# Performance work log

Measured on AMD Instinct MI355X. Metric: run time of the kernel, lower is better.

Reference implementation:

```python
import jax, jax.numpy as jnp
import numpy as np

B, M, N, F, H = 4, 512, 1024, 256, 256
K, K2, KC, RADIUS = 8, 4, 16, 0.5
EPS = 1e-5


def _cdist(a, b):
    d2 = (jnp.sum(a * a, -1)[..., :, None] + jnp.sum(b * b, -1)[..., None, :]
          - 2.0 * jnp.einsum('bnd,bmd->bnm', a, b))
    return jnp.sqrt(jnp.maximum(d2, 0.0))


def _scf_oe(xyz):
    # spherical coords (r, theta, phi) relative to cloud centroid -> (B,3,Npts)
    rel = xyz - jnp.mean(xyz, axis=1, keepdims=True)
    r = jnp.sqrt(jnp.sum(rel * rel, -1) + 1e-8)
    theta = jnp.arccos(jnp.clip(rel[..., 2] / r, -1.0, 1.0))
    phi = jnp.arctan2(rel[..., 1], rel[..., 0])
    return jnp.stack([r, theta, phi], axis=1)


def _knn_desc(xyz):
    # per-point SCF descriptor: sorted distances to KC nearest neighbors
    d = _cdist(xyz, xyz)
    return jnp.sort(d, axis=-1)[..., 1:KC + 1]


def _inorm(x):
    # InstanceNorm1d, affine=False: normalize over last dim per (b, row)
    mu = jnp.mean(x, -1, keepdims=True)
    var = jnp.var(x, -1, keepdims=True)
    return (x - mu) / jnp.sqrt(var + EPS)


def _conv1x1(x, W, g, b):
    # Conv2d 1x1 + BN(affine) + ReLU on (B,C,N,K)
    y = jnp.einsum('bcnk,oc->bonk', x, W)
    return jax.nn.relu(g[:, None, None] * y + b[:, None, None])


def _conv12(x, W, g, b):
    # Conv2d kernel (1,2) stride (1,2) + BN(affine) + ReLU on (B,C,N,P)
    Bb, C, Nn, P = x.shape
    xr = x.reshape(Bb, C, Nn, P // 2, 2)
    y = jnp.einsum('bcnpt,oct->bonp', xr, W)
    return jax.nn.relu(g[:, None, None] * y + b[:, None, None])


def _pointsift(xyz, feat, params):
    # PointSIFT OE: nearest neighbor in each of 8 octants within radius
    w1, g1, b1, w2, g2, b2, w3, g3, b3 = params
    Bb, Nn, _ = xyz.shape
    diff = xyz[:, None, :, :] - xyz[:, :, None, :]  # diff[b,i,j] = xyz[j]-xyz[i]
    d2 = jnp.sum(diff * diff, -1)
    octant = ((diff[..., 0] > 0).astype(jnp.int32) * 4
              + (diff[..., 1] > 0).astype(jnp.int32) * 2
              + (diff[..., 2] > 0).astype(jnp.int32))
    base = jnp.broadcast_to(jnp.arange(Nn)[None, :], (Bb, Nn))
    idxs = []
    for c in range(8):  # fixed small structural loop
        m = (octant == c) & (d2 <= RADIUS * RADIUS) & (d2 > 0)
        dm = jnp.where(m, d2, jnp.inf)
        j = jnp.argmin(dm, -1)
        valid = jnp.isfinite(jnp.min(dm, -1))
        idxs.append(jnp.where(valid, j, base))
    idx = jnp.stack(idxs, -1)  # (B,N,8)
    gxyz = jax.vmap(lambda p, i: p[i])(xyz, idx) - xyz[:, :, None, :]
    gfeat = jax.vmap(lambda f, i: f[i])(feat, idx)
    g = jnp.concatenate([gxyz, gfeat], -1).transpose(0, 3, 1, 2)  # (B,3+C,N,8)
    g = _conv12(g, w1, g1, b1)
    g = _conv12(g, w2, g2, b2)
    g = _conv12(g, w3, g3, b3)
    return g[..., 0]  # (B,C,N)


def setup_inputs():
    key = jax.random.key(0)
    ks = iter(jax.random.split(key, 64))
    rn = lambda shape, s=0.05: jax.random.normal(next(ks), shape, dtype=jnp.float32) * s
    ones = lambda shape: jnp.ones(shape, jnp.float32)
    zeros = lambda shape: jnp.zeros(shape, jnp.float32)
    inp = {
        'template_feature': rn((B, F, M), 1.0),
        'search_feature': rn((B, F, N), 1.0),
        'template_xyz': rn((B, M, 3), 1.0),
        'search_xyz': rn((B, N, 3), 1.0),
        'template_bc': rn((B, M, 9), 1.0),
        'search_bc': rn((B, N, 9), 1.0),
        'mlp_w1': rn((H, F + 3)), 'mlp_g1': ones(H), 'mlp_b1': zeros(H),
        'mlp_w2': rn((H, H)), 'mlp_g2': ones(H), 'mlp_b2': zeros(H),
        'mlp_w3': rn((H, H)), 'mlp_g3': ones(H), 'mlp_b3': zeros(H),
        'fea_w1': rn((F, H)), 'fea_g1': ones(F), 'fea_b1': zeros(F),
        'fea_w2': rn((F, F)), 'fea_bias2': zeros(F),
        'attn_wqkv': rn((3 * F, F)),
        'pos_w1': rn((64, 12)), 'pos_b1': zeros(64),
        'pos_w2': rn((F, 64)), 'pos_b2': zeros(F),
        'amlp_w1': rn((4 * F, F)), 'amlp_b1': zeros(4 * F),
        'amlp_w2': rn((F, 4 * F)), 'amlp_b2': zeros(F),
        'oe1_w1': rn((F, F + 3, 2)), 'oe1_g1': ones(F), 'oe1_b1': zeros(F),
        'oe1_w2': rn((F, F, 2)), 'oe1_g2': ones(F), 'oe1_b2': zeros(F),
        'oe1_w3': rn((F, F, 2)), 'oe1_g3': ones(F), 'oe1_b3': zeros(F),
        'oe2_w1': rn((F, F + 3, 2)), 'oe2_g1': ones(F), 'oe2_b1': zeros(F),
        'oe2_w2': rn((F, F, 2)), 'oe2_g2': ones(F), 'oe2_b2': zeros(F),
        'oe2_w3': rn((F, F, 2)), 'oe2_g3': ones(F), 'oe2_b3': zeros(F),
    }
    return inp


def reference(template_feature, search_feature, template_xyz, search_xyz, template_bc, search_bc,
              mlp_w1, mlp_g1, mlp_b1, mlp_w2, mlp_g2, mlp_b2, mlp_w3, mlp_g3, mlp_b3,
              fea_w1, fea_g1, fea_b1, fea_w2, fea_bias2,
              attn_wqkv, pos_w1, pos_b1, pos_w2, pos_b2, amlp_w1, amlp_b1, amlp_w2, amlp_b2,
              oe1_w1, oe1_g1, oe1_b1, oe1_w2, oe1_g2, oe1_b2, oe1_w3, oe1_g3, oe1_b3,
              oe2_w1, oe2_g1, oe2_b1, oe2_w2, oe2_g2, oe2_b2, oe2_w3, oe2_g3, oe2_b3):
    # ---- box-cloud distance + candidate pruning ----
    dist_bc = _cdist(template_bc, search_bc)  # (B,M,N)
    t_box = jnp.concatenate([template_xyz.transpose(0, 2, 1), template_bc.transpose(0, 2, 1),
                             template_feature, _scf_oe(template_xyz)], 1)  # (B,15+F,M)
    s_box = jnp.concatenate([search_xyz.transpose(0, 2, 1), search_bc.transpose(0, 2, 1),
                             search_feature, _scf_oe(search_xyz)], 1)      # (B,15+F,N)
    idx_b = jnp.argsort(dist_bc, axis=1)[:, :3 * K, :].transpose(0, 2, 1)  # (B,N,3K)
    dist_xyz = _cdist(search_xyz, template_xyz)  # (B,N,M)
    bi = jnp.arange(B)[:, None, None]
    ni = jnp.arange(N)[None, :, None]
    mask = jnp.full((B, N, M), 1e5, jnp.float32).at[bi, ni, idx_b].set(1.0)
    idx_k = jnp.argsort((dist_xyz * mask).transpose(0, 2, 1), axis=1)[:, :K, :].transpose(0, 2, 1)  # (B,N,K)
    # ---- SCF descriptor matching restricted to xyz candidates ----
    sd = _knn_desc(search_xyz)
    td = _knn_desc(template_xyz)
    mask2 = jnp.full((B, N, M), 1e5, jnp.float32).at[bi, ni, idx_k].set(1.0)
    dist_scf = _cdist(sd, td) * mask2
    idx_s = jnp.argsort(dist_scf.transpose(0, 2, 1), axis=1)[:, :K2, :].transpose(0, 2, 1)  # (B,N,K2)
    # ---- grouping + shared MLP ----
    corr = jax.vmap(lambda f, i: f[:, i])(t_box, idx_s)        # (B,15+F,N,K2)
    fused = jnp.concatenate([s_box[..., None], corr], -1)      # (B,15+F,N,K2+1)
    feats = fused.transpose(0, 2, 3, 1)[..., 12:]              # drop xyz+bc -> (B,N,K2+1,F+3)
    h = feats.transpose(0, 3, 1, 2)
    h = _conv1x1(h, mlp_w1, mlp_g1, mlp_b1)
    h = _conv1x1(h, mlp_w2, mlp_g2, mlp_b2)
    h = _conv1x1(h, mlp_w3, mlp_g3, mlp_b3)
    h = h.transpose(0, 2, 3, 1)                                # (B,N,K2+1,H)
    nn_xyz = corr[:, 0:3].transpose(0, 2, 3, 1)
    st_xyz = jnp.concatenate([search_xyz[:, :, None, :], nn_xyz], 2)
    nn_bc = corr[:, 3:12].transpose(0, 2, 3, 1)
    st_bc = jnp.concatenate([search_bc[:, :, None, :], nn_bc], 2)
    pos = jnp.concatenate([st_xyz, st_bc], -1)                 # (B,N,K2+1,12)
    KP1 = K2 + 1
    x = h.reshape(B * N, KP1, H)
    p = pos.reshape(B * N, KP1, 12)
    # ---- point transformer layer over tiny neighborhoods ----
    qkv = jnp.einsum('bnd,ed->bne', x, attn_wqkv)
    q, k, v = jnp.split(qkv, 3, axis=-1)
    rel_pos = p[:, :, None, :] - p[:, None, :, :]
    pe = jnp.einsum('bijp,hp->bijh', rel_pos, pos_w1) + pos_b1
    pe = jnp.einsum('bijh,dh->bijd', jax.nn.relu(pe), pos_w2) + pos_b2
    sim_in = q[:, :, None, :] - k[:, None, :, :] + pe
    hh = jax.nn.relu(jnp.einsum('bijd,hd->bijh', sim_in, amlp_w1) + amlp_b1)
    sim = jnp.einsum('bijh,dh->bijd', hh, amlp_w2) + amlp_b2
    attn = jax.nn.softmax(sim, axis=-2)
    agg = jnp.einsum('bijd,bijd->bid', attn, v[:, None, :, :] + pe)
    ff = agg.reshape(B, N, KP1, H).transpose(0, 3, 1, 2)[..., 0]  # (B,F,N)
    # ---- residual + instance norms + fea_layer ----
    ff = ff + search_feature
    ff = _inorm(ff.transpose(0, 2, 1)).transpose(0, 2, 1)
    y = jax.nn.relu(fea_g1[:, None] * jnp.einsum('bcn,oc->bon', ff, fea_w1) + fea_b1[:, None])
    y = jnp.einsum('bcn,oc->bon', y, fea_w2) + fea_bias2[:, None]
    y = _inorm((y + ff).transpose(0, 2, 1)).transpose(0, 2, 1)
    # ---- two PointSIFT OE modules with residuals ----
    y = y + _pointsift(search_xyz, y.transpose(0, 2, 1), (oe1_w1, oe1_g1, oe1_b1, oe1_w2, oe1_g2, oe1_b2, oe1_w3, oe1_g3, oe1_b3))
    y = y + _pointsift(search_xyz, y.transpose(0, 2, 1), (oe2_w1, oe2_g1, oe2_b1, oe2_w2, oe2_g2, oe2_b2, oe2_w3, oe2_g3, oe2_b3))
    return y
```

## Files before the change

kernel.cpp:

```cpp
#include <hip/hip_runtime.h>
#include <hip/hip_bf16.h>
#include <math.h>

constexpr int Bc = 4, Mc = 512, Nc = 1024, Fc = 256;
constexpr int KCc = 16;
constexpr float INFF = 3.0e38f;

typedef __attribute__((ext_vector_type(8))) short short8b;
typedef __attribute__((ext_vector_type(4))) float f32x4;

__device__ __forceinline__ short f2bf(float f) {
  __hip_bfloat16 h = __float2bfloat16(f);
  return *reinterpret_cast<short*>(&h);
}
__device__ __forceinline__ float bf2f(short s) {
  unsigned int u = ((unsigned int)(unsigned short)s) << 16;
  return __uint_as_float(u);
}
__device__ __forceinline__ unsigned long long umin64(unsigned long long a, unsigned long long b) {
  return a < b ? a : b;
}

__device__ __forceinline__ float blk_sum(float v, float* red) {
  int t = threadIdx.x;
// ... 73 lines not shown
  float mx = blk_sum(sx, red) / (float)P;
  float my = blk_sum(sy, red) / (float)P;
  float mz = blk_sum(sz, red) / (float)P;
  for (int i = threadIdx.x; i < P; i += 256) {
    float a = x[3 * i] - mx, c = x[3 * i + 1] - my, d = x[3 * i + 2] - mz;
    float r = sqrtf(a * a + c * c + d * d + 1e-8f);
    float ct = d / r;
    ct = fminf(1.f, fmaxf(-1.f, ct));
    out[((size_t)b * 3 + 0) * P + i] = r;
    out[((size_t)b * 3 + 1) * P + i] = acosf(ct);
    out[((size_t)b * 3 + 2) * P + i] = atan2f(c, a);
  }
}

template <int P>
__global__ __launch_bounds__(256) void knn_kernel(const float* __restrict__ xyz,
                                                  float* __restrict__ desc) {
  constexpr int E = P / 64;
  int wv = threadIdx.x >> 6, l = threadIdx.x & 63;
  int pt = blockIdx.x * 4 + wv;
  int b = pt / P, i = pt % P;
  const float* x = xyz + (size_t)b * P * 3;
  float xi0 = x[3 * i], xi1 = x[3 * i + 1], xi2 = x[3 * i + 2];
  float d2r[E];
#pragma unroll
  for (int q = 0; q < E; ++q) {
    int j = q * 64 + l;
    float dx = x[3 * j] - xi0, dy = x[3 * j + 1] - xi1, dz = x[3 * j + 2] - xi2;
    d2r[q] = dx * dx + dy * dy + dz * dz;
  }
  for (int round = 0; round < KCc + 1; ++round) {
    unsigned long long k = ~0ULL;
#pragma unroll
    for (int q = 0; q < E; ++q) {
      unsigned long long c =
          ((unsigned long long)__float_as_uint(d2r[q]) << 32) | (unsigned)(q * 64 + l);
      k = umin64(k, c);
    }
#pragma unroll
    for (int m = 1; m < 64; m <<= 1) k = umin64(k, __shfl_xor(k, m));
    int widx = (int)(unsigned)k;
    if (round > 0 && l == 0)
      desc[((size_t)b * P + i) * KCc + (round - 1)] = sqrtf(__uint_as_float((unsigned)(k >> 32)));
    if ((widx & 63) == l) {
      int q = widx >> 6;
#pragma unroll
      for (int qq = 0; qq < E; ++qq)
        if (qq == q) d2r[qq] = INFF;
    }
  }
}

__global__ __launch_bounds__(256) void select_kernel(
    const float* __restrict__ tbc, const float* __restrict__ sbc,
    const float* __restrict__ txyz, const float* __restrict__ sxyz,
    const float* __restrict__ sd, const float* __restrict__ td,
    int* __restrict__ idx_s) {
  __shared__ int cand4[4][24];
  int wv = threadIdx.x >> 6, l = threadIdx.x & 63;
  int pt = blockIdx.x * 4 + wv;
  int b = pt / Nc, n = pt % Nc;
  const float* sb = sbc + ((size_t)b * Nc + n) * 9;
  float sreg[9];
#pragma unroll
  for (int c = 0; c < 9; ++c) sreg[c] = sb[c];
  float d2r[8];
#pragma unroll
  for (int q = 0; q < 8; ++q) {
    int m = q * 64 + l;
    const float* tb = tbc + ((size_t)b * Mc + m) * 9;
    float acc = 0.f;
#pragma unroll
    for (int c = 0; c < 9; ++c) { float d = tb[c] - sreg[c]; acc += d * d; }
    d2r[q] = acc;
  }
  for (int round = 0; round < 24; ++round) {
    unsigned long long k = ~0ULL;
#pragma unroll
    for (int q = 0; q < 8; ++q) {
      unsigned long long c =
          ((unsigned long long)__float_as_uint(d2r[q]) << 32) | (unsigned)(q * 64 + l);
      k = umin64(k, c);
    }
#pragma unroll
    for (int m = 1; m < 64; m <<= 1) k = umin64(k, __shfl_xor(k, m));
    int widx = (int)(unsigned)k;
    if (l == 0) cand4[wv][round] = widx;
    if ((widx & 63) == l) {
      int q = widx >> 6;
#pragma unroll
      for (int qq = 0; qq < 8; ++qq)
        if (qq == q) d2r[qq] = INFF;
    }
  }
  if (l == 0) {
    int* cand = cand4[wv];
    const float* sp = sxyz + ((size_t)b * Nc + n) * 3;
    float sx = sp[0], sy = sp[1], sz = sp[2];
    float dv[24];
    for (int t2 = 0; t2 < 24; ++t2) {
      const float* tp = txyz + ((size_t)b * Mc + cand[t2]) * 3;
      float dx = tp[0] - sx, dy = tp[1] - sy, dz = tp[2] - sz;
      dv[t2] = dx * dx + dy * dy + dz * dz;
    }
    int c8[8]; bool used[24];
    for (int t2 = 0; t2 < 24; ++t2) used[t2] = false;
    for (int r = 0; r < 8; ++r) {
      float bv = INFF; int bt = -1, bm = 0x7fffffff;
      for (int t2 = 0; t2 < 24; ++t2) {
        if (used[t2]) continue;
        int m = cand[t2];
        if (bt < 0 || dv[t2] < bv || (dv[t2] == bv && m < bm)) { bv = dv[t2]; bt = t2; bm = m; }
      }
      used[bt] = true; c8[r] = bm;
    }
    const float* sdp = sd + ((size_t)b * Nc + n) * KCc;
    float sdr[16];
    for (int t2 = 0; t2 < 16; ++t2) sdr[t2] = sdp[t2];
    float dscf[8];
    for (int r = 0; r < 8; ++r) {
      const float* tdp = td + ((size_t)b * Mc + c8[r]) * KCc;
      float acc = 0.f;
      for (int t2 = 0; t2 < 16; ++t2) { float d = sdr[t2] - tdp[t2]; acc += d * d; }
      dscf[r] = acc;
    }
    bool u8[8] = {false, false, false, false, false, false, false, false};
    for (int r = 0; r < 4; ++r) {
      float bv = INFF; int bt = -1, bm = 0x7fffffff;
      for (int t2 = 0; t2 < 8; ++t2) {
        if (u8[t2]) continue;
        if (bt < 0 || dscf[t2] < bv || (dscf[t2] == bv && c8[t2] < bm)) { bv = dscf[t2]; bt = t2; bm = c8[t2]; }
      }
      u8[bt] = true;
      idx_s[(((size_t)b * Nc + n) << 2) + r] = bm;
    }
  }
}

__global__ __launch_bounds__(512, 4) void mlp_attn_kernel(
    const float* __restrict__ sfeatT, const float* __restrict__ tfeatT,
    const float* __restrict__ sscf, const float* __restrict__ tscf,
    const int* __restrict__ idx_s,
    const short* __restrict__ mw1f, const float* __restrict__ mg1, const float* __restrict__ mb1,
    const short* __restrict__ mw2f, const float* __restrict__ mg2, const float* __restrict__ mb2,
    const short* __restrict__ mw3f, const float* __restrict__ mg3, const float* __restrict__ mb3,
    const float* __restrict__ sxyz, const float* __restrict__ sbc,
    const float* __restrict__ txyz, const float* __restrict__ tbc,
    const short* __restrict__ aqf, const short* __restrict__ akpef, const short* __restrict__ avpef,
    const float* __restrict__ pw1, const float* __restrict__ pb1, const float* __restrict__ pb2,
    const short* __restrict__ aw1f, const float* __restrict__ ab1,
    const short* __restrict__ aw2f, const float* __restrict__ ab2,
    const short* __restrict__ fw1f, const float* __restrict__ fg1, const float* __restrict__ fb1,
    const short* __restrict__ fw2f, const float* __restrict__ fb2v,
    float* __restrict__ yout) {
  __shared__ __align__(16) char smem[79872];
  char* mB1 = smem;
  char* mB2 = smem + 27648;
  char* mB3 = smem + 52224;
  char* Bx   = smem;
  char* vpeB = smem;
  char* feaB = smem;
  char* feaH = smem + 8192;
  float* y2F = (float*)(smem + 16384);
  char* KB   = smem + 30720;
  char* simS = smem + 30720;
  char* HpB  = smem + 55296;
  float* qF  = (float*)(smem + 55296);
  float* q04 = (float*)(smem + 55296);
  float* redf = (float*)(smem + 63488);
  float* pc4 = (float*)(smem + 64000);
  __shared__ int ms[32];
  int t = threadIdx.x;
  int tau0 = blockIdx.x * 8;
  int b = tau0 / Nc, n0 = tau0 % Nc;
  int w = t >> 6, l = t & 63, lg = l >> 4, lr = l & 15;
  int h = t >> 8, ch = t & 255;
  if (t < 32) ms[t] = idx_s[(((size_t)b * Nc + n0 + (t >> 2)) << 2) + (t & 3)];
  __syncthreads();
  for (int z = t; z < 48 * 29; z += 512) {
    int col = z / 29, k = 259 + z % 29;
    *(short*)(mB1 + ((col * 576 + 2 * k) ^ ((col & 7) << 4))) = 0;
  }
  for (int z = t; z < 8 * 259; z += 512) {
    int col = 40 + z / 259, k = z % 259;
    *(short*)(mB1 + ((col * 576 + 2 * k) ^ ((col & 7) << 4))) = 0;
  }
  for (int sj = h; sj < 40; sj += 2) {
    int s = sj / 5, j = sj % 5;
    int n = n0 + s;
    int cx = (sj & 7) << 4;
    if (j == 0) {
      *(short*)(mB1 + ((sj * 576 + 2 * ch) ^ cx)) =
          f2bf(sfeatT[((size_t)b * Nc + n) * 256 + ch]);
      if (ch < 3)
        *(short*)(mB1 + ((sj * 576 + (256 + ch) * 2) ^ cx)) = f2bf(sscf[((size_t)b * 3 + ch) * Nc + n]);
    } else {
      int m = ms[s * 4 + j - 1];
      *(short*)(mB1 + ((sj * 576 + 2 * ch) ^ cx)) =
          f2bf(tfeatT[((size_t)b * Mc + m) * 256 + ch]);
      if (ch < 3)
        *(short*)(mB1 + ((sj * 576 + (256 + ch) * 2) ^ cx)) = f2bf(tscf[((size_t)b * 3 + ch) * Mc + m]);
    }
  }
  __syncthreads();
  {
    f32x4 acc[2][3];
#pragma unroll
    for (int i = 0; i < 2; ++i)
#pragma unroll
      for (int ct = 0; ct < 3; ++ct) acc[i][ct] = (f32x4){0,0,0,0};
    for (int kk = 0; kk < 9; ++kk) {
      short8b bb[3];
#pragma unroll
      for (int ct = 0; ct < 3; ++ct) {
        int col = ct * 16 + lr;
        bb[ct] = *(const short8b*)(mB1 + ((col * 576 + kk * 64 + lg * 16) ^ ((col & 7) << 4)));
      }
#pragma unroll
      for (int i = 0; i < 2; ++i) {
        short8b a = *(const short8b*)(mw1f + (((size_t)((w * 2 + i) * 9 + kk)) * 64 + l) * 8);
#pragma unroll
        for (int ct = 0; ct < 3; ++ct)
          acc[i][ct] = __builtin_amdgcn_mfma_f32_16x16x32_bf16(a, bb[ct], acc[i][ct], 0, 0, 0);
      }
    }
    __syncthreads();
#pragma unroll
    for (int i = 0; i < 2; ++i) {
      int r0 = (w * 2 + i) * 16 + lg * 4;
      float4 gg = *(const float4*)(mg1 + r0), bs = *(const float4*)(mb1 + r0);
#pragma unroll
      for (int ct = 0; ct < 3; ++ct) {
        int col = ct * 16 + lr; int cx = (col & 7) << 4;
        ushort4 hv;
        hv.x = (unsigned short)f2bf(fmaxf(gg.x * acc[i][ct][0] + bs.x, 0.f));
        hv.y = (unsigned short)f2bf(fmaxf(gg.y * acc[i][ct][1] + bs.y, 0.f));
        hv.z = (unsigned short)f2bf(fmaxf(gg.z * acc[i][ct][2] + bs.z, 0.f));
        hv.w = (unsigned short)f2bf(fmaxf(gg.w * acc[i][ct][3] + bs.w, 0.f));
        *(ushort4*)(mB2 + ((col * 512 + r0 * 2) ^ cx)) = hv;
      }
    }
  }
  __syncthreads();
  {
    f32x4 acc[2][3];
#pragma unroll
    for (int i = 0; i < 2; ++i)
#pragma unroll
      for (int ct = 0; ct < 3; ++ct) acc[i][ct] = (f32x4){0,0,0,0};
    for (int kk = 0; kk < 8; ++kk) {
      short8b bb[3];
#pragma unroll
      for (int ct = 0; ct < 3; ++ct) {
        int col = ct * 16 + lr;
        bb[ct] = *(const short8b*)(mB2 + ((col * 512 + kk * 64 + lg * 16) ^ ((col & 7) << 4)));
      }
#pragma unroll
      for (int i = 0; i < 2; ++i) {
        short8b a = *(const short8b*)(mw2f + (((size_t)((w * 2 + i) * 8 + kk)) * 64 + l) * 8);
#pragma unroll
        for (int ct = 0; ct < 3; ++ct)
          acc[i][ct] = __builtin_amdgcn_mfma_f32_16x16x32_bf16(a, bb[ct], acc[i][ct], 0, 0, 0);
      }
    }
    __syncthreads();
#pragma unroll
    for (int i = 0; i < 2; ++i) {
      int r0 = (w * 2 + i) * 16 + lg * 4;
      float4 gg = *(const float4*)(mg2 + r0), bs = *(const float4*)(mb2 + r0);
#pragma unroll
      for (int ct = 0; ct < 3; ++ct) {
        int col = ct * 16 + lr; int cx = (col & 7) << 4;
        ushort4 hv;
        hv.x = (unsigned short)f2bf(fmaxf(gg.x * acc[i][ct][0] + bs.x, 0.f));
        hv.y = (unsigned short)f2bf(fmaxf(gg.y * acc[i][ct][1] + bs.y, 0.f));
        hv.z = (unsigned short)f2bf(fmaxf(gg.z * acc[i][ct][2] + bs.z, 0.f));
        hv.w = (unsigned short)f2bf(fmaxf(gg.w * acc[i][ct][3] + bs.w, 0.f));
        *(ushort4*)(mB3 + ((col * 512 + r0 * 2) ^ cx)) = hv;
      }
    }
  }
  __syncthreads();
  {
    f32x4 acc[2][3];
#pragma unroll
    for (int i = 0; i < 2; ++i)
#pragma unroll
      for (int ct = 0; ct < 3; ++ct) acc[i][ct] = (f32x4){0,0,0,0};
    for (int kk = 0; kk < 8; ++kk) {
      short8b bb[3];
#pragma unroll
      for (int ct = 0; ct < 3; ++ct) {
        int col = ct * 16 + lr;
        bb[ct] = *(const short8b*)(mB3 + ((col * 512 + kk * 64 + lg * 16) ^ ((col & 7) << 4)));
      }
#pragma unroll
      for (int i = 0; i < 2; ++i) {
        short8b a = *(const short8b*)(mw3f + (((size_t)((w * 2 + i) * 8 + kk)) * 64 + l) * 8);
#pragma unroll
        for (int ct = 0; ct < 3; ++ct)
          acc[i][ct] = __builtin_amdgcn_mfma_f32_16x16x32_bf16(a, bb[ct], acc[i][ct], 0, 0, 0);
      }
    }
    __syncthreads();
#pragma unroll
    for (int i = 0; i < 2; ++i) {
      int r0 = (w * 2 + i) * 16 + lg * 4;
      float4 gg = *(const float4*)(mg3 + r0), bs = *(const float4*)(mb3 + r0);
#pragma unroll
      for (int ct = 0; ct < 3; ++ct) {
        int col = ct * 16 + lr;
        if (col < 40) {
          int cx = (col & 7) << 4;
          ushort4 hv;
          hv.x = (unsigned short)f2bf(fmaxf(gg.x * acc[i][ct][0] + bs.x, 0.f));
          hv.y = (unsigned short)f2bf(fmaxf(gg.y * acc[i][ct][1] + bs.y, 0.f));
          hv.z = (unsigned short)f2bf(fmaxf(gg.z * acc[i][ct][2] + bs.z, 0.f));
          hv.w = (unsigned short)f2bf(fmaxf(gg.w * acc[i][ct][3] + bs.w, 0.f));
          *(ushort4*)(Bx + ((col * 640 + r0 * 2) ^ cx)) = hv;
        }
      }
    }
    for (int z = t; z < 2560; z += 512) {
      int col = 40 + z / 320, k = z % 320;
      *(short*)(Bx + ((col * 640 + 2 * k) ^ ((col & 7) << 4))) = 0;
    }
  }
  __syncthreads();
  if (t < 40) {
    int s = t / 5, k = t % 5;
    int n = n0 + s;
    float* pd = pc4 + t * 12;
    if (k == 0) {
      for (int c = 0; c < 3; ++c) pd[c] = sxyz[((size_t)b * Nc + n) * 3 + c];
      for (int c = 0; c < 9; ++c) pd[3 + c] = sbc[((size_t)b * Nc + n) * 9 + c];
    } else {
      int m = idx_s[(((size_t)b * Nc + n) << 2) + (k - 1)];
      for (int c = 0; c < 3; ++c) pd[c] = txyz[((size_t)b * Mc + m) * 3 + c];
      for (int c = 0; c < 9; ++c) pd[3 + c] = tbc[((size_t)b * Mc + m) * 9 + c];
    }
  }
  __syncthreads();
  for (int it = t; it < 2560; it += 512) {
    int sj = it >> 6, hh = it & 63;
    int s = sj / 5;
    float acc = pb1[hh];
    const float* wv = pw1 + hh * 12;
    const float* p0 = pc4 + (s * 5) * 12;
    const float* pj = pc4 + sj * 12;
#pragma unroll
    for (int p = 0; p < 12; ++p) acc += wv[p] * (p0[p] - pj[p]);
    *(short*)(Bx + ((sj * 640 + 512 + 2 * hh) ^ ((sj & 7) << 4))) = f2bf(fmaxf(acc, 0.f));
  }
  __syncthreads();
  {
    f32x4 qA[2][3];
#pragma unroll
    for (int i = 0; i < 2; ++i)
#pragma unroll
      for (int ct = 0; ct < 3; ++ct) qA[i][ct] = (f32x4){0,0,0,0};
    for (int kk = 0; kk < 8; ++kk) {
      short8b bq[3];
#pragma unroll
      for (int ct = 0; ct < 3; ++ct) {
        int col = ct * 16 + lr;
        bq[ct] = *(const short8b*)(Bx + ((col * 640 + kk * 64 + lg * 16) ^ ((col & 7) << 4)));
      }
#pragma unroll
      for (int i = 0; i < 2; ++i) {
        short8b a = *(const short8b*)(aqf + (((size_t)((w * 2 + i) * 8 + kk)) * 64 + l) * 8);
#pragma unroll
        for (int ct = 0; ct < 3; ++ct)
          qA[i][ct] = __builtin_amdgcn_mfma_f32_16x16x32_bf16(a, bq[ct], qA[i][ct], 0, 0, 0);
      }
    }
#pragma unroll
    for (int i = 0; i < 2; ++i) {
      int r0 = (w * 2 + i) * 16 + lg * 4;
#pragma unroll
      for (int ct = 0; ct < 3; ++ct) {
        int col = ct * 16 + lr;
        if (col < 40 && col % 5 == 0)
          *(f32x4*)(qF + (col / 5) * 256 + r0) = qA[i][ct];
      }
    }
  }
  f32x4 sA[2][3], vA[2][3];
#pragma unroll
  for (int i = 0; i < 2; ++i)
#pragma unroll
    for (int ct = 0; ct < 3; ++ct) { sA[i][ct] = (f32x4){0,0,0,0}; vA[i][ct] = (f32x4){0,0,0,0}; }
  for (int kk = 0; kk < 10; ++kk) {
    short8b bb[3];
#pragma unroll
    for (int ct = 0; ct < 3; ++ct) {
      int col = ct * 16 + lr;
      bb[ct] = *(const short8b*)(Bx + ((col * 640 + kk * 64 + lg * 16) ^ ((col & 7) << 4)));
    }
#pragma unroll
    for (int i = 0; i < 2; ++i) {
      short8b ak = *(const short8b*)(akpef + (((size_t)((w * 2 + i) * 10 + kk)) * 64 + l) * 8);
      short8b av = *(const short8b*)(avpef + (((size_t)((w * 2 + i) * 10 + kk)) * 64 + l) * 8);
#pragma unroll
      for (int ct = 0; ct < 3; ++ct) {
        sA[i][ct] = __builtin_amdgcn_mfma_f32_16x16x32_bf16(ak, bb[ct], sA[i][ct], 0, 0, 0);
        vA[i][ct] = __builtin_amdgcn_mfma_f32_16x16x32_bf16(av, bb[ct], vA[i][ct], 0, 0, 0);
      }
    }
  }
  __syncthreads();
#pragma unroll
  for (int i = 0; i < 2; ++i) {
    int r0 = (w * 2 + i) * 16 + lg * 4;
    float4 pb = *(const float4*)(pb2 + r0);
#pragma unroll
    for (int ct = 0; ct < 3; ++ct) {
      int col = ct * 16 + lr; int cx = (col & 7) << 4;
      if (col < 40) {
        int s = col / 5;
        f32x4 qv = *(const f32x4*)(qF + s * 256 + r0);
        ushort4 kv, vv;
        kv.x = (unsigned short)f2bf(qv[0] + sA[i][ct][0] + pb.x);
        kv.y = (unsigned short)f2bf(qv[1] + sA[i][ct][1] + pb.y);
        kv.z = (unsigned short)f2bf(qv[2] + sA[i][ct][2] + pb.z);
        kv.w = (unsigned short)f2bf(qv[3] + sA[i][ct][3] + pb.w);
        vv.x = (unsigned short)f2bf(vA[i][ct][0] + pb.x);
        vv.y = (unsigned short)f2bf(vA[i][ct][1] + pb.y);
        vv.z = (unsigned short)f2bf(vA[i][ct][2] + pb.z);
        vv.w = (unsigned short)f2bf(vA[i][ct][3] + pb.w);
        *(ushort4*)(KB + ((col * 512 + r0 * 2) ^ cx)) = kv;
        *(ushort4*)(vpeB + ((col * 512 + r0 * 2) ^ cx)) = vv;
      } else {
        ushort4 zz; zz.x = zz.y = zz.z = zz.w = 0;
        *(ushort4*)(KB + ((col * 512 + r0 * 2) ^ cx)) = zz;
      }
    }
  }
  __syncthreads();
  f32x4 sacc[2][3];
#pragma unroll
  for (int i = 0; i < 2; ++i)
#pragma unroll
    for (int ct = 0; ct < 3; ++ct) sacc[i][ct] = (f32x4){0,0,0,0};
  for (int p = 0; p < 4; ++p) {
    f32x4 hacc[2][3];
#pragma unroll
    for (int i = 0; i < 2; ++i)
#pragma unroll
      for (int ct = 0; ct < 3; ++ct) hacc[i][ct] = (f32x4){0,0,0,0};
    for (int kk = 0; kk < 8; ++kk) {
      short8b bb[3];
#pragma unroll
      for (int ct = 0; ct < 3; ++ct) {
        int col = ct * 16 + lr;
        bb[ct] = *(const short8b*)(KB + ((col * 512 + kk * 64 + lg * 16) ^ ((col & 7) << 4)));
      }
#pragma unroll
      for (int i = 0; i < 2; ++i) {
        int rtg = p * 16 + w * 2 + i;
        short8b a = *(const short8b*)(aw1f + (((size_t)(rtg * 8 + kk)) * 64 + l) * 8);
#pragma unroll
        for (int ct = 0; ct < 3; ++ct)
          hacc[i][ct] = __builtin_amdgcn_mfma_f32_16x16x32_bf16(a, bb[ct], hacc[i][ct], 0, 0, 0);
      }
    }
#pragma unroll
    for (int i = 0; i < 2; ++i) {
      int r0l = (w * 2 + i) * 16 + lg * 4;
      float4 bias = *(const float4*)(ab1 + p * 256 + r0l);
#pragma unroll
      for (int ct = 0; ct < 3; ++ct) {
        int col = ct * 16 + lr; int cx = (col & 7) << 4;
        ushort4 hv;
        hv.x = (unsigned short)f2bf(fmaxf(hacc[i][ct][0] + bias.x, 0.f));
        hv.y = (unsigned short)f2bf(fmaxf(hacc[i][ct][1] + bias.y, 0.f));
        hv.z = (unsigned short)f2bf(fmaxf(hacc[i][ct][2] + bias.z, 0.f));
        hv.w = (unsigned short)f2bf(fmaxf(hacc[i][ct][3] + bias.w, 0.f));
        *(ushort4*)(HpB + ((col * 512 + r0l * 2) ^ cx)) = hv;
      }
    }
    __syncthreads();
    for (int kk = 0; kk < 8; ++kk) {
      short8b bb[3];
#pragma unroll
      for (int ct = 0; ct < 3; ++ct) {
        int col = ct * 16 + lr;
        bb[ct] = *(const short8b*)(HpB + ((col * 512 + kk * 64 + lg * 16) ^ ((col & 7) << 4)));
      }
      int kkg = p * 8 + kk;
#pragma unroll
      for (int i = 0; i < 2; ++i) {
        short8b a = *(const short8b*)(aw2f + (((size_t)((w * 2 + i) * 32 + kkg)) * 64 + l) * 8);
#pragma unroll
        for (int ct = 0; ct < 3; ++ct)
          sacc[i][ct] = __builtin_amdgcn_mfma_f32_16x16x32_bf16(a, bb[ct], sacc[i][ct], 0, 0, 0);
      }
    }
    __syncthreads();
  }
#pragma unroll
  for (int i = 0; i < 2; ++i) {
    int r0 = (w * 2 + i) * 16 + lg * 4;
    float4 bias = *(const float4*)(ab2 + r0);
#pragma unroll
    for (int ct = 0; ct < 3; ++ct) {
      int col = ct * 16 + lr;
      if (col < 40) {
        ushort4 hv;
        hv.x = (unsigned short)f2bf(sacc[i][ct][0] + bias.x);
        hv.y = (unsigned short)f2bf(sacc[i][ct][1] + bias.y);
        hv.z = (unsigned short)f2bf(sacc[i][ct][2] + bias.z);
        hv.w = (unsigned short)f2bf(sacc[i][ct][3] + bias.w);
        *(ushort4*)(simS + col * 528 + r0 * 2) = hv;
      }
    }
  }
  __syncthreads();
  float ffv[4];
#pragma unroll
  for (int si = 0; si < 4; ++si) {
    int s = h * 4 + si;
    float sv[5], vp[5];
#pragma unroll
    for (int j = 0; j < 5; ++j) {
      int sj = s * 5 + j;
      sv[j] = bf2f(*(const short*)(simS + sj * 528 + 2 * ch));
      vp[j] = bf2f(*(const short*)(vpeB + ((sj * 512 + 2 * ch) ^ ((sj & 7) << 4))));
    }
    float mx = sv[0];
#pragma unroll
    for (int j = 1; j < 5; ++j) mx = fmaxf(mx, sv[j]);
    float ssum = 0.f;
#pragma unroll
    for (int j = 0; j < 5; ++j) { sv[j] = expf(sv[j] - mx); ssum += sv[j]; }
    float inv = 1.f / ssum;
    float agg = 0.f;
#pragma unroll
    for (int j = 0; j < 5; ++j) agg += (sv[j] * inv) * vp[j];
    ffv[si] = agg + sfeatT[((size_t)b * Nc + (n0 + s)) * 256 + ch];
  }
  {
    float rv[8];
#pragma unroll
    for (int si = 0; si < 4; ++si) { rv[si] = ffv[si]; rv[4 + si] = ffv[si] * ffv[si]; }
#pragma unroll
    for (int m = 1; m < 64; m <<= 1)
#pragma unroll
      for (int i2 = 0; i2 < 8; ++i2) rv[i2] += __shfl_xor(rv[i2], m);
    if ((t & 63) == 0)
#pragma unroll
      for (int i2 = 0; i2 < 8; ++i2) redf[w * 8 + i2] = rv[i2];
    __syncthreads();
#pragma unroll
    for (int si = 0; si < 4; ++si) {
      int s = h * 4 + si;
      float S = 0.f, Q = 0.f;
#pragma unroll
      for (int q2 = 0; q2 < 4; ++q2) {
        S += redf[(h * 4 + q2) * 8 + si];
        Q += redf[(h * 4 + q2) * 8 + 4 + si];
      }
      float mu = S * (1.f / 256.f);
      float var = Q * (1.f / 256.f) - mu * mu;
      q04[s * 256 + ch] = (ffv[si] - mu) / sqrtf(var + 1e-5f);
    }
  }
  __syncthreads();
  for (int z = t; z < 16 * 256; z += 512) {
    int col = z >> 8, k = z & 255;
    short val = (col < 8) ? f2bf(q04[col * 256 + k]) : (short)0;
    *(short*)(feaB + ((col * 512 + 2 * k) ^ ((col & 7) << 4))) = val;
  }
  __syncthreads();
  {
    f32x4 acc[2];
#pragma unroll
    for (int i = 0; i < 2; ++i) acc[i] = (f32x4){0,0,0,0};
    for (int kk = 0; kk < 8; ++kk) {
      short8b b0 = *(const short8b*)(feaB + ((lr * 512 + kk * 64 + lg * 16) ^ ((lr & 7) << 4)));
#pragma unroll
      for (int i = 0; i < 2; ++i) {
        short8b a = *(const short8b*)(fw1f + (((size_t)((w * 2 + i) * 8 + kk)) * 64 + l) * 8);
        acc[i] = __builtin_amdgcn_mfma_f32_16x16x32_bf16(a, b0, acc[i], 0, 0, 0);
      }
    }
#pragma unroll
    for (int i = 0; i < 2; ++i) {
      int r0 = (w * 2 + i) * 16 + lg * 4;
      float4 gg = *(const float4*)(fg1 + r0), bs = *(const float4*)(fb1 + r0);
      int cx = (lr & 7) << 4;
      ushort4 hv;
      hv.x = (unsigned short)f2bf(fmaxf(gg.x * acc[i][0] + bs.x, 0.f));
      hv.y = (unsigned short)f2bf(fmaxf(gg.y * acc[i][1] + bs.y, 0.f));
      hv.z = (unsigned short)f2bf(fmaxf(gg.z * acc[i][2] + bs.z, 0.f));
      hv.w = (unsigned short)f2bf(fmaxf(gg.w * acc[i][3] + bs.w, 0.f));
      *(ushort4*)(feaH + ((lr * 512 + r0 * 2) ^ cx)) = hv;
    }
  }
  __syncthreads();
  {
    f32x4 acc[2];
#pragma unroll
    for (int i = 0; i < 2; ++i) acc[i] = (f32x4){0,0,0,0};
    for (int kk = 0; kk < 8; ++kk) {
      short8b b0 = *(const short8b*)(feaH + ((lr * 512 + kk * 64 + lg * 16) ^ ((lr & 7) << 4)));
#pragma unroll
      for (int i = 0; i < 2; ++i) {
        short8b a = *(const short8b*)(fw2f + (((size_t)((w * 2 + i) * 8 + kk)) * 64 + l) * 8);
        acc[i] = __builtin_amdgcn_mfma_f32_16x16x32_bf16(a, b0, acc[i], 0, 0, 0);
      }
    }
#pragma unroll
    for (int i = 0; i < 2; ++i) {
      if (lr < 8) {
        int r0 = (w * 2 + i) * 16 + lg * 4;
        float4 bs = *(const float4*)(fb2v + r0);
        float4 v;
        v.x = acc[i][0] + bs.x; v.y = acc[i][1] + bs.y;
        v.z = acc[i][2] + bs.z; v.w = acc[i][3] + bs.w;
        *(float4*)(y2F + lr * 260 + r0) = v;
      }
    }
  }
  __syncthreads();
  {
    float zv[4];
#pragma unroll
    for (int si = 0; si < 4; ++si) {
      int s = h * 4 + si;
      zv[si] = y2F[s * 260 + ch] + q04[s * 256 + ch];
    }
    float rv[8];
#pragma unroll
    for (int si = 0; si < 4; ++si) { rv[si] = zv[si]; rv[4 + si] = zv[si] * zv[si]; }
#pragma unroll
    for (int m = 1; m < 64; m <<= 1)
#pragma unroll
      for (int i2 = 0; i2 < 8; ++i2) rv[i2] += __shfl_xor(rv[i2], m);
    if ((t & 63) == 0)
#pragma unroll
      for (int i2 = 0; i2 < 8; ++i2) redf[w * 8 + i2] = rv[i2];
    __syncthreads();
#pragma unroll
    for (int si = 0; si < 4; ++si) {
      int s = h * 4 + si;
      float S = 0.f, Q = 0.f;
#pragma unroll
      for (int q2 = 0; q2 < 4; ++q2) {
        S += redf[(h * 4 + q2) * 8 + si];
        Q += redf[(h * 4 + q2) * 8 + 4 + si];
      }
      float mu = S * (1.f / 256.f);
      float var = Q * (1.f / 256.f) - mu * mu;
      yout[((size_t)(tau0 + s)) * 256 + ch] = (zv[si] - mu) / sqrtf(var + 1e-5f);
    }
  }
}

__global__ __launch_bounds__(256) void sift_idx_kernel(const float* __restrict__ sxyz,
                                                       int* __restrict__ sidx) {
  int wv = threadIdx.x >> 6, l = threadIdx.x & 63;
  int pt = blockIdx.x * 4 + wv;
  int b = pt / Nc, i = pt % Nc;
  const float* x = sxyz + (size_t)b * Nc * 3;
  float xi0 = x[3 * i], xi1 = x[3 * i + 1], xi2 = x[3 * i + 2];
  unsigned long long k8[8];
#pragma unroll
  for (int o = 0; o < 8; ++o) k8[o] = ~0ULL;
  for (int q = 0; q < 16; ++q) {
    int j = q * 64 + l;
    float dx = x[3 * j] - xi0, dy = x[3 * j + 1] - xi1, dz = x[3 * j + 2] - xi2;
    float d2 = dx * dx + dy * dy + dz * dz;
    bool ok = (d2 <= 0.25f) && (d2 > 0.f);
    int oc = (dx > 0.f ? 4 : 0) + (dy > 0.f ? 2 : 0) + (dz > 0.f ? 1 : 0);
    unsigned long long c = ((unsigned long long)__float_as_uint(d2) << 32) | (unsigned)j;
#pragma unroll
    for (int o = 0; o < 8; ++o) {
      unsigned long long cc = (ok && oc == o) ? c : ~0ULL;
      k8[o] = umin64(k8[o], cc);
    }
  }
#pragma unroll
  for (int m = 1; m < 64; m <<= 1)
#pragma unroll
    for (int o = 0; o < 8; ++o) k8[o] = umin64(k8[o], __shfl_xor(k8[o], m));
  if (l < 8) {
    unsigned long long r = ~0ULL;
#pragma unroll
    for (int o = 0; o < 8; ++o)
      if (l == o) r = k8[o];
    int j = (r == ~0ULL) ? i : (int)(unsigned)r;
    sidx[(((size_t)b * Nc + i) << 3) + l] = j;
  }
}

__global__ __launch_bounds__(512, 4) void sift_oe_kernel(
    const float* __restrict__ sxyz, const int* __restrict__ sidx,
    const float* __restrict__ yin,
    const short* __restrict__ w1f, const float* __restrict__ g1, const float* __restrict__ b1,
    const short* __restrict__ w2f, const float* __restrict__ g2, const float* __restrict__ b2,
    const short* __restrict__ w3f, const float* __restrict__ g3, const float* __restrict__ b3,
    float* __restrict__ yout) {
  __shared__ __align__(16) char smem[51200];
  char* B1 = smem;
  char* B2 = smem + 34816;
  char* B3 = smem;
  __shared__ int js[8][8];
  int t = threadIdx.x;
  int i0 = blockIdx.x * 8;
  int b = i0 / Nc, nb = i0 % Nc;
  int h = t >> 8, ch = t & 255;
  if (t < 64) js[t >> 3][t & 7] = sidx[(((size_t)b * Nc + nb + (t >> 3)) << 3) + (t & 7)];
  for (int z = t; z < 32 * 26; z += 512) {
    int col = z / 26, k = 518 + z % 26;
    *(short*)(B1 + ((col * 1088 + 2 * k) ^ ((col & 7) << 4))) = 0;
  }
  __syncthreads();
  for (int si = 0; si < 4; ++si) {
    int s = h * 4 + si;
    int ii = nb + s;
#pragma unroll
    for (int p = 0; p < 4; ++p) {
      int ja = js[s][2 * p], jb = js[s][2 * p + 1];
      int col = s * 4 + p; int cx = (col & 7) << 4;
      float va = yin[((size_t)b * Nc + ja) * 256 + ch];
      float vb = yin[((size_t)b * Nc + jb) * 256 + ch];
      unsigned int packed = (unsigned int)(unsigned short)f2bf(va) |
                            ((unsigned int)(unsigned short)f2bf(vb) << 16);
      *(unsigned int*)(B1 + ((col * 1088 + 12 + 4 * ch) ^ cx)) = packed;
      if (ch < 3) {
        float base = sxyz[((size_t)b * Nc + ii) * 3 + ch];
        float ga = sxyz[((size_t)b * Nc + ja) * 3 + ch] - base;
        float gb = sxyz[((size_t)b * Nc + jb) * 3 + ch] - base;
        unsigned int pg = (unsigned int)(unsigned short)f2bf(ga) |
                          ((unsigned int)(unsigned short)f2bf(gb) << 16);
        *(unsigned int*)(B1 + ((col * 1088 + 4 * ch) ^ cx)) = pg;
      }
    }
  }
  __syncthreads();
  int l = t & 63, w = t >> 6, lg = l >> 4, lr = l & 15;
  {
    f32x4 acc[2][2];
#pragma unroll
    for (int i = 0; i < 2; ++i) { acc[i][0] = (f32x4){0,0,0,0}; acc[i][1] = (f32x4){0,0,0,0}; }
    for (int kk = 0; kk < 17; ++kk) {
      short8b b0[2];
#pragma unroll
      for (int ct = 0; ct < 2; ++ct) {
        int col = ct * 16 + lr;
        b0[ct] = *(const short8b*)(B1 + ((col * 1088 + kk * 64 + lg * 16) ^ ((col & 7) << 4)));
      }
#pragma unroll
      for (int i = 0; i < 2; ++i) {
        short8b a = *(const short8b*)(w1f + (((size_t)((w * 2 + i) * 17 + kk)) * 64 + l) * 8);
#pragma unroll
        for (int ct = 0; ct < 2; ++ct)
          acc[i][ct] = __builtin_amdgcn_mfma_f32_16x16x32_bf16(a, b0[ct], acc[i][ct], 0, 0, 0);
      }
    }
    __syncthreads();
#pragma unroll
    for (int i = 0; i < 2; ++i) {
      int r0 = (w * 2 + i) * 16 + lg * 4;
// ... 4 lines not shown
        int s = col >> 2, p = col & 3, p2 = p >> 1, tp = p & 1;
        int col2 = s * 2 + p2; int cx2 = (col2 & 7) << 4;
        *(short*)(B2 + ((col2 * 1024 + (2 * r0 + tp) * 2) ^ cx2)) =
            f2bf(fmaxf(gg.x * acc[i][ct][0] + bs.x, 0.f));
        *(short*)(B2 + ((col2 * 1024 + (2 * (r0 + 1) + tp) * 2) ^ cx2)) =
            f2bf(fmaxf(gg.y * acc[i][ct][1] + bs.y, 0.f));
        *(short*)(B2 + ((col2 * 1024 + (2 * (r0 + 2) + tp) * 2) ^ cx2)) =
            f2bf(fmaxf(gg.z * acc[i][ct][2] + bs.z, 0.f));
        *(short*)(B2 + ((col2 * 1024 + (2 * (r0 + 3) + tp) * 2) ^ cx2)) =
            f2bf(fmaxf(gg.w * acc[i][ct][3] + bs.w, 0.f));
      }
    }
  }
  __syncthreads();
  {
    f32x4 acc[2];
#pragma unroll
    for (int i = 0; i < 2; ++i) acc[i] = (f32x4){0,0,0,0};
    for (int kk = 0; kk < 16; ++kk) {
      short8b b0 = *(const short8b*)(B2 + ((lr * 1024 + kk * 64 + lg * 16) ^ ((lr & 7) << 4)));
#pragma unroll
      for (int i = 0; i < 2; ++i) {
        short8b a = *(const short8b*)(w2f + (((size_t)((w * 2 + i) * 16 + kk)) * 64 + l) * 8);
        acc[i] = __builtin_amdgcn_mfma_f32_16x16x32_bf16(a, b0, acc[i], 0, 0, 0);
      }
    }
    __syncthreads();
    int s = lr >> 1, tp = lr & 1;
    int col3 = s; int cx3 = (col3 & 7) << 4;
#pragma unroll
    for (int i = 0; i < 2; ++i) {
      int r0 = (w * 2 + i) * 16 + lg * 4;
      float4 gg = *(const float4*)(g2 + r0), bs = *(const float4*)(b2 + r0);
      *(short*)(B3 + ((col3 * 1024 + (2 * r0 + tp) * 2) ^ cx3)) =
          f2bf(fmaxf(gg.x * acc[i][0] + bs.x, 0.f));
      *(short*)(B3 + ((col3 * 1024 + (2 * (r0 + 1) + tp) * 2) ^ cx3)) =
          f2bf(fmaxf(gg.y * acc[i][1] + bs.y, 0.f));
      *(short*)(B3 + ((col3 * 1024 + (2 * (r0 + 2) + tp) * 2) ^ cx3)) =
          f2bf(fmaxf(gg.z * acc[i][2] + bs.z, 0.f));
      *(short*)(B3 + ((col3 * 1024 + (2 * (r0 + 3) + tp) * 2) ^ cx3)) =
          f2bf(fmaxf(gg.w * acc[i][3] + bs.w, 0.f));
    }
  }
  __syncthreads();
  {
    f32x4 acc[2];
#pragma unroll
    for (int i = 0; i < 2; ++i) acc[i] = (f32x4){0,0,0,0};
    for (int kk = 0; kk < 16; ++kk) {
      short8b b0 = *(const short8b*)(B3 + ((lr * 1024 + kk * 64 + lg * 16) ^ ((lr & 7) << 4)));
#pragma unroll
      for (int i = 0; i < 2; ++i) {
        short8b a = *(const short8b*)(w3f + (((size_t)((w * 2 + i) * 16 + kk)) * 64 + l) * 8);
        acc[i] = __builtin_amdgcn_mfma_f32_16x16x32_bf16(a, b0, acc[i], 0, 0, 0);
      }
    }
#pragma unroll
    for (int i = 0; i < 2; ++i) {
      if (lr < 8) {
        int s = lr;
        int r0 = (w * 2 + i) * 16 + lg * 4;
        float4 gg = *(const float4*)(g3 + r0), bs = *(const float4*)(b3 + r0);
        float4 yv = *(const float4*)(yin + ((size_t)(i0 + s)) * 256 + r0);
        float4 ov;
        ov.x = yv.x + fmaxf(gg.x * acc[i][0] + bs.x, 0.f);
        ov.y = yv.y + fmaxf(gg.y * acc[i][1] + bs.y, 0.f);
        ov.z = yv.z + fmaxf(gg.z * acc[i][2] + bs.z, 0.f);
        ov.w = yv.w + fmaxf(gg.w * acc[i][3] + bs.w, 0.f);
        *(float4*)(yout + ((size_t)(i0 + s)) * 256 + r0) = ov;
      }
    }
  }
}

extern "C" void kernel_launch(void* const* d_in, const int* in_sizes, int n_in,
                              void* d_out, int out_size, void* d_ws, size_t ws_size,
                              hipStream_t stream) {
  (void)in_sizes; (void)n_in; (void)out_size; (void)ws_size;
  const float* tfeat = (const float*)d_in[0];
  const float* sfeat = (const float*)d_in[1];
  const float* txyz  = (const float*)d_in[2];
  const float* sxyz  = (const float*)d_in[3];
  const float* tbc   = (const float*)d_in[4];
  const float* sbc   = (const float*)d_in[5];
  const float* mw1 = (const float*)d_in[6];
  const float* mg1 = (const float*)d_in[7];
  const float* mb1 = (const float*)d_in[8];
  const float* mw2 = (const float*)d_in[9];
  const float* mg2 = (const float*)d_in[10];
  const float* mb2 = (const float*)d_in[11];
  const float* mw3 = (const float*)d_in[12];
  const float* mg3 = (const float*)d_in[13];
  const float* mb3 = (const float*)d_in[14];
  const float* fw1 = (const float*)d_in[15];
  const float* fg1 = (const float*)d_in[16];
  const float* fb1 = (const float*)d_in[17];
  const float* fw2 = (const float*)d_in[18];
  const float* fb2 = (const float*)d_in[19];
  const float* wqkv = (const float*)d_in[20];
  const float* pw1 = (const float*)d_in[21];
  const float* pb1 = (const float*)d_in[22];
  const float* pw2 = (const float*)d_in[23];
  const float* pb2 = (const float*)d_in[24];
  const float* aw1 = (const float*)d_in[25];
  const float* ab1 = (const float*)d_in[26];
  const float* aw2 = (const float*)d_in[27];
  const float* ab2 = (const float*)d_in[28];
  const float* o1w1 = (const float*)d_in[29];
  const float* o1g1 = (const float*)d_in[30];
  const float* o1b1 = (const float*)d_in[31];
  const float* o1w2 = (const float*)d_in[32];
  const float* o1g2 = (const float*)d_in[33];
  const float* o1b2 = (const float*)d_in[34];
  const float* o1w3 = (const float*)d_in[35];
  const float* o1g3 = (const float*)d_in[36];
  const float* o1b3 = (const float*)d_in[37];
  const float* o2w1 = (const float*)d_in[38];
  const float* o2g1 = (const float*)d_in[39];
  const float* o2b1 = (const float*)d_in[40];
  const float* o2w2 = (const float*)d_in[41];
  const float* o2g2 = (const float*)d_in[42];
  const float* o2b2 = (const float*)d_in[43];
  const float* o2w3 = (const float*)d_in[44];
  const float* o2g3 = (const float*)d_in[45];
  const float* o2b3 = (const float*)d_in[46];

  float* ws = (float*)d_ws;
  float* sd   = ws;
  float* td   = sd + 65536;
  float* sscf = td + 32768;
  float* tscf = sscf + 12288;
  int*   idxs = (int*)(tscf + 6144);
  int*   sidx = idxs + 16384;
  float* yws  = (float*)(sidx + 32768);
  short* sb   = (short*)(yws + 1048576);
  short* mw1f  = sb + 5242880;
  short* mw2f  = mw1f + 73728;
  short* mw3f  = mw2f + 65536;
  short* aqf   = mw3f + 65536;
  short* akpef = aqf + 65536;
  short* avpef = akpef + 81920;
  short* aw1f  = avpef + 81920;
  short* aw2f  = aw1f + 262144;
  short* fw1f  = aw2f + 262144;
  short* fw2f  = fw1f + 65536;
  short* o1w1f = fw2f + 65536;
  short* o1w2f = o1w1f + 139264;
  short* o1w3f = o1w2f + 131072;
  short* o2w1f = o1w3f + 131072;
  short* o2w2f = o2w1f + 139264;
  short* o2w3f = o2w2f + 131072;
  float* sfeatT = (float*)(sb + 7135232);
  float* tfeatT = sfeatT + 1048576;
  float* ybuf2 = (float*)sb;

  WSrcs srcs;
  srcs.p[0] = mw1;  srcs.p[1] = mw2;  srcs.p[2] = mw3;  srcs.p[3] = wqkv;
  srcs.p[4] = wqkv; srcs.p[5] = wqkv; srcs.p[6] = aw1;  srcs.p[7] = aw2;
  srcs.p[8] = fw1;  srcs.p[9] = fw2;  srcs.p[10] = o1w1; srcs.p[11] = o1w2;
  srcs.p[12] = o1w3; srcs.p[13] = o2w1; srcs.p[14] = o2w2; srcs.p[15] = o2w3;
  wconv_all<<<7392, 256, 0, stream>>>(srcs, pw2, mw1f);

  transpose_any<<<Bc * 4 * 16, 256, 0, stream>>>(sfeat, sfeatT, Fc, Nc);
  transpose_any<<<Bc * 4 * 8, 256, 0, stream>>>(tfeat, tfeatT, Fc, Mc);

  scf_kernel<<<Bc, 256, 0, stream>>>(sxyz, sscf, Nc);
  scf_kernel<<<Bc, 256, 0, stream>>>(txyz, tscf, Mc);
  knn_kernel<Nc><<<Bc * Nc / 4, 256, 0, stream>>>(sxyz, sd);
  knn_kernel<Mc><<<Bc * Mc / 4, 256, 0, stream>>>(txyz, td);
  select_kernel<<<Bc * Nc / 4, 256, 0, stream>>>(tbc, sbc, txyz, sxyz, sd, td, idxs);
  mlp_attn_kernel<<<Bc * Nc / 8, 512, 0, stream>>>(
      sfeatT, tfeatT, sscf, tscf, idxs,
      mw1f, mg1, mb1, mw2f, mg2, mb2, mw3f, mg3, mb3,
      sxyz, sbc, txyz, tbc,
      aqf, akpef, avpef, pw1, pb1, pb2,
      aw1f, ab1, aw2f, ab2,
      fw1f, fg1, fb1, fw2f, fb2, yws);
  sift_idx_kernel<<<Bc * Nc / 4, 256, 0, stream>>>(sxyz, sidx);
  sift_oe_kernel<<<Bc * Nc / 8, 512, 0, stream>>>(sxyz, sidx, yws,
                                                  o1w1f, o1g1, o1b1, o1w2f, o1g2, o1b2,
                                                  o1w3f, o1g3, o1b3, ybuf2);
  sift_oe_kernel<<<Bc * Nc / 8, 512, 0, stream>>>(sxyz, sidx, ybuf2,
                                                  o2w1f, o2g1, o2b1, o2w2f, o2g2, o2b2,
                                                  o2w3f, o2g3, o2b3, yws);
  transpose_any<<<Bc * 16 * 4, 256, 0, stream>>>(yws, (float*)d_out, Nc, Fc);
}
```

Baseline: 319.5 us.

## Shrink attention kernel LDS by spilling V+PE to global scratch and reusing buffers

Repacks the mlp_attn_kernel shared-memory map, cutting LDS from about 78KB to 52KB so more 512-thread blocks can be resident per CU. The V+PE tile is moved out of LDS into a per-block global scratch region, and the padding columns 40-47 are no longer zeroed or written. Extra barriers are added where buffers now alias. In exchange it adds global-memory round trips for the V+PE values and depends on those padding columns never being read in a way that affects the result.

Result: slower. 326.7 us (+2.3%).

```diff
diff --git a/kernel.cpp b/kernel.cpp
--- a/kernel.cpp
+++ b/kernel.cpp
@@ -249,37 +249,34 @@
     const short* __restrict__ aw2f, const float* __restrict__ ab2,
     const short* __restrict__ fw1f, const float* __restrict__ fg1, const float* __restrict__ fb1,
     const short* __restrict__ fw2f, const float* __restrict__ fb2v,
+    short* __restrict__ vpeG,
     float* __restrict__ yout) {
-  __shared__ __align__(16) char smem[79872];
+  __shared__ __align__(16) char smem[53248];
   char* mB1 = smem;
-  char* mB2 = smem + 27648;
-  char* mB3 = smem + 52224;
-  char* Bx   = smem;
-  char* vpeB = smem;
-  char* feaB = smem;
-  char* feaH = smem + 8192;
-  float* y2F = (float*)(smem + 16384);
-  char* KB   = smem + 30720;
-  char* simS = smem + 30720;
-  char* HpB  = smem + 55296;
-  float* qF  = (float*)(smem + 55296);
-  float* q04 = (float*)(smem + 55296);
-  float* redf = (float*)(smem + 63488);
-  float* pc4 = (float*)(smem + 64000);
-  __shared__ int ms[32];
+  char* mB2 = smem + 23040;
+  char* mB3 = smem;
+  char* Bx  = smem + 20480;
+  float* qF = (float*)smem;
+  char* KB  = smem + 8192;
+  char* HpB = smem + 28672;
+  char* simS = smem;
+  float* q04 = (float*)(smem + 21120);
+  char* feaB = smem + 29312;
+  char* feaH = smem + 37504;
+  float* y2F = (float*)smem;
+  float* pc4 = (float*)(smem + 49152);
+  float* redf = (float*)(smem + 51072);
+  int* ms = (int*)(smem + 51584);
   int t = threadIdx.x;
   int tau0 = blockIdx.x * 8;
   int b = tau0 / Nc, n0 = tau0 % Nc;
   int w = t >> 6, l = t & 63, lg = l >> 4, lr = l & 15;
   int h = t >> 8, ch = t & 255;
+  short* vpeL = vpeG + (size_t)blockIdx.x * 10240;
   if (t < 32) ms[t] = idx_s[(((size_t)b * Nc + n0 + (t >> 2)) << 2) + (t & 3)];
   __syncthreads();
-  for (int z = t; z < 48 * 29; z += 512) {
+  for (int z = t; z < 40 * 29; z += 512) {
     int col = z / 29, k = 259 + z % 29;
-    *(short*)(mB1 + ((col * 576 + 2 * k) ^ ((col & 7) << 4))) = 0;
-  }
-  for (int z = t; z < 8 * 259; z += 512) {
-    int col = 40 + z / 259, k = z % 259;
     *(short*)(mB1 + ((col * 576 + 2 * k) ^ ((col & 7) << 4))) = 0;
   }
   for (int sj = h; sj < 40; sj += 2) {
@@ -328,13 +325,16 @@
       float4 gg = *(const float4*)(mg1 + r0), bs = *(const float4*)(mb1 + r0);
 #pragma unroll
       for (int ct = 0; ct < 3; ++ct) {
-        int col = ct * 16 + lr; int cx = (col & 7) << 4;
-        ushort4 hv;
-        hv.x = (unsigned short)f2bf(fmaxf(gg.x * acc[i][ct][0] + bs.x, 0.f));
-        hv.y = (unsigned short)f2bf(fmaxf(gg.y * acc[i][ct][1] + bs.y, 0.f));
-        hv.z = (unsigned short)f2bf(fmaxf(gg.z * acc[i][ct][2] + bs.z, 0.f));
-        hv.w = (unsigned short)f2bf(fmaxf(gg.w * acc[i][ct][3] + bs.w, 0.f));
-        *(ushort4*)(mB2 + ((col * 512 + r0 * 2) ^ cx)) = hv;
+        int col = ct * 16 + lr;
+        if (col < 40) {
+          int cx = (col & 7) << 4;
+          ushort4 hv;
+          hv.x = (unsigned short)f2bf(fmaxf(gg.x * acc[i][ct][0] + bs.x, 0.f));
+          hv.y = (unsigned short)f2bf(fmaxf(gg.y * acc[i][ct][1] + bs.y, 0.f));
+          hv.z = (unsigned short)f2bf(fmaxf(gg.z * acc[i][ct][2] + bs.z, 0.f));
+          hv.w = (unsigned short)f2bf(fmaxf(gg.w * acc[i][ct][3] + bs.w, 0.f));
+          *(ushort4*)(mB2 + ((col * 512 + r0 * 2) ^ cx)) = hv;
+        }
       }
     }
   }
@@ -367,13 +367,16 @@
       float4 gg = *(const float4*)(mg2 + r0), bs = *(const float4*)(mb2 + r0);
 #pragma unroll
       for (int ct = 0; ct < 3; ++ct) {
-        int col = ct * 16 + lr; int cx = (col & 7) << 4;
-        ushort4 hv;
-        hv.x = (unsigned short)f2bf(fmaxf(gg.x * acc[i][ct][0] + bs.x, 0.f));
-        hv.y = (unsigned short)f2bf(fmaxf(gg.y * acc[i][ct][1] + bs.y, 0.f));
-        hv.z = (unsigned short)f2bf(fmaxf(gg.z * acc[i][ct][2] + bs.z, 0.f));
-        hv.w = (unsigned short)f2bf(fmaxf(gg.w * acc[i][ct][3] + bs.w, 0.f));
-        *(ushort4*)(mB3 + ((col * 512 + r0 * 2) ^ cx)) = hv;
+        int col = ct * 16 + lr;
+        if (col < 40) {
+          int cx = (col & 7) << 4;
+          ushort4 hv;
+          hv.x = (unsigned short)f2bf(fmaxf(gg.x * acc[i][ct][0] + bs.x, 0.f));
+          hv.y = (unsigned short)f2bf(fmaxf(gg.y * acc[i][ct][1] + bs.y, 0.f));
+          hv.z = (unsigned short)f2bf(fmaxf(gg.z * acc[i][ct][2] + bs.z, 0.f));
+          hv.w = (unsigned short)f2bf(fmaxf(gg.w * acc[i][ct][3] + bs.w, 0.f));
+          *(ushort4*)(mB3 + ((col * 512 + r0 * 2) ^ cx)) = hv;
+        }
       }
     }
   }
@@ -417,10 +420,6 @@
           *(ushort4*)(Bx + ((col * 640 + r0 * 2) ^ cx)) = hv;
         }
       }
-    }
-    for (int z = t; z < 2560; z += 512) {
-      int col = 40 + z / 320, k = z % 320;
-      *(short*)(Bx + ((col * 640 + 2 * k) ^ ((col & 7) << 4))) = 0;
     }
   }
   __syncthreads();
@@ -512,8 +511,9 @@
     float4 pb = *(const float4*)(pb2 + r0);
 #pragma unroll
     for (int ct = 0; ct < 3; ++ct) {
-      int col = ct * 16 + lr; int cx = (col & 7) << 4;
+      int col = ct * 16 + lr;
       if (col < 40) {
+        int cx = (col & 7) << 4;
         int s = col / 5;
         f32x4 qv = *(const f32x4*)(qF + s * 256 + r0);
         ushort4 kv, vv;
@@ -526,10 +526,7 @@
         vv.z = (unsigned short)f2bf(vA[i][ct][2] + pb.z);
         vv.w = (unsigned short)f2bf(vA[i][ct][3] + pb.w);
         *(ushort4*)(KB + ((col * 512 + r0 * 2) ^ cx)) = kv;
-        *(ushort4*)(vpeB + ((col * 512 + r0 * 2) ^ cx)) = vv;
-      } else {
-        ushort4 zz; zz.x = zz.y = zz.z = zz.w = 0;
-        *(ushort4*)(KB + ((col * 512 + r0 * 2) ^ cx)) = zz;
+        *(ushort4*)(vpeL + col * 256 + r0) = vv;
       }
     }
   }
@@ -561,19 +558,23 @@
           hacc[i][ct] = __builtin_amdgcn_mfma_f32_16x16x32_bf16(a, bb[ct], hacc[i][ct], 0, 0, 0);
       }
     }
+    __syncthreads();
 #pragma unroll
     for (int i = 0; i < 2; ++i) {
       int r0l = (w * 2 + i) * 16 + lg * 4;
       float4 bias = *(const float4*)(ab1 + p * 256 + r0l);
 #pragma unroll
       for (int ct = 0; ct < 3; ++ct) {
-        int col = ct * 16 + lr; int cx = (col & 7) << 4;
-        ushort4 hv;
-        hv.x = (unsigned short)f2bf(fmaxf(hacc[i][ct][0] + bias.x, 0.f));
-        hv.y = (unsigned short)f2bf(fmaxf(hacc[i][ct][1] + bias.y, 0.f));
-        hv.z = (unsigned short)f2bf(fmaxf(hacc[i][ct][2] + bias.z, 0.f));
-        hv.w = (unsigned short)f2bf(fmaxf(hacc[i][ct][3] + bias.w, 0.f));
-        *(ushort4*)(HpB + ((col * 512 + r0l * 2) ^ cx)) = hv;
+        int col = ct * 16 + lr;
+        if (col < 40) {
+          int cx = (col & 7) << 4;
+          ushort4 hv;
+          hv.x = (unsigned short)f2bf(fmaxf(hacc[i][ct][0] + bias.x, 0.f));
+          hv.y = (unsigned short)f2bf(fmaxf(hacc[i][ct][1] + bias.y, 0.f));
+          hv.z = (unsigned short)f2bf(fmaxf(hacc[i][ct][2] + bias.z, 0.f));
+          hv.w = (unsigned short)f2bf(fmaxf(hacc[i][ct][3] + bias.w, 0.f));
+          *(ushort4*)(HpB + ((col * 512 + r0l * 2) ^ cx)) = hv;
+        }
       }
     }
     __syncthreads();
@@ -622,7 +623,7 @@
     for (int j = 0; j < 5; ++j) {
       int sj = s * 5 + j;
       sv[j] = bf2f(*(const short*)(simS + sj * 528 + 2 * ch));
-      vp[j] = bf2f(*(const short*)(vpeB + ((sj * 512 + 2 * ch) ^ ((sj & 7) << 4))));
+      vp[j] = bf2f(vpeL[sj * 256 + ch]);
     }
     float mx = sv[0];
 #pragma unroll
@@ -707,6 +708,7 @@
         acc[i] = __builtin_amdgcn_mfma_f32_16x16x32_bf16(a, b0, acc[i], 0, 0, 0);
       }
     }
+    __syncthreads();
 #pragma unroll
     for (int i = 0; i < 2; ++i) {
       if (lr < 8) {
@@ -1017,6 +1019,7 @@
   short* o2w3f = o2w2f + 131072;
   float* sfeatT = (float*)(sb + 7135232);
   float* tfeatT = sfeatT + 1048576;
+  short* vpeG  = sb;
   float* ybuf2 = (float*)sb;
 
   WSrcs srcs;
@@ -1040,7 +1043,7 @@
       sxyz, sbc, txyz, tbc,
       aqf, akpef, avpef, pw1, pb1, pb2,
       aw1f, ab1, aw2f, ab2,
-      fw1f, fg1, fb1, fw2f, fb2, yws);
+      fw1f, fg1, fb1, fw2f, fb2, vpeG, yws);
   sift_idx_kernel<<<Bc * Nc / 4, 256, 0, stream>>>(sxyz, sidx);
   sift_oe_kernel<<<Bc * Nc / 8, 512, 0, stream>>>(sxyz, sidx, yws,
                                                   o1w1f, o1g1, o1b1, o1w2f, o1g2, o1b2,
```
